# Kernel optimization log

Hardware: AMD Instinct MI355X
Metric: run time of the kernel (lower is better)

The kernel has to match this reference:

```python
import jax, jax.numpy as jnp
import numpy as np


def setup_inputs() -> dict:
    key = jax.random.key(0)
    x = jax.random.normal(key, (16, 64, 256, 256), dtype=jnp.float32)
    return {"x": x}


def reference(x):
    # x: [B, C, H, W]
    b, c, h, w = x.shape
    # L2 norm over channel dim -> [B, 1, H, W]
    weights = jnp.sqrt(jnp.sum(x * x, axis=1, keepdims=True))
    # softmax over height (dim=2)
    weights = jax.nn.softmax(weights, axis=2)
    # weighted sum over height -> [B, C, 1, W]
    weighted_sum = jnp.sum(x * weights, axis=2, keepdims=True)
    weight_sum = jnp.sum(weights, axis=2, keepdims=True)  # [B, 1, 1, W]
    compressed = weighted_sum / (weight_sum + 1e-8)
    # broadcast-repeat along height -> [B, C, H, W]
    out = jnp.broadcast_to(compressed, (b, c, h, w))
    return out
```

## Files before the change

kernel.cpp:

```cpp
#include <hip/hip_runtime.h>


constexpr int B = 16, C = 64, H = 256, W = 256, W4 = 64;
constexpr int HC = 32;
constexpr int HPC = H / HC;
constexpr float KSUB = 8.0f;

typedef float nfloat4 __attribute__((ext_vector_type(4)));

__device__ __forceinline__ float4 f4add(float4 a, float4 b) {
    return make_float4(a.x + b.x, a.y + b.y, a.z + b.z, a.w + b.w);
}

__global__ __launch_bounds__(512, 4) void k_pass1(const float* __restrict__ x,
                                                  float4* __restrict__ pcomp,
                                                  float4* __restrict__ pden) {
    __shared__ float4 red[2][8][64];
    int blk = blockIdx.x;
    int b = blk >> 5, hc = blk & 31;
    int t = threadIdx.x, cg = t >> 6, w4 = t & 63;
    int h0 = hc * HPC;

    const float4* xb = (const float4*)x + ((size_t)(b * C + cg * 8) * H + h0) * W4 + w4;

    float4 acc[8];
#pragma unroll
    for (int j = 0; j < 8; ++j) acc[j] = make_float4(0.f, 0.f, 0.f, 0.f);
    float4 dacc = make_float4(0.f, 0.f, 0.f, 0.f);

    for (int hh = 0; hh < HPC; ++hh) {
        float4 xv[8];
        float4 ps = make_float4(0.f, 0.f, 0.f, 0.f);
#pragma unroll
        for (int j = 0; j < 8; ++j) {
            xv[j] = xb[(size_t)j * H * W4 + (size_t)hh * W4];
            ps.x += xv[j].x * xv[j].x; ps.y += xv[j].y * xv[j].y;
            ps.z += xv[j].z * xv[j].z; ps.w += xv[j].w * xv[j].w;
        }
        red[hh & 1][cg][w4] = ps;
        __syncthreads();
        float4 s = make_float4(0.f, 0.f, 0.f, 0.f);
#pragma unroll
        for (int g = 0; g < 8; ++g) s = f4add(s, red[hh & 1][g][w4]);
        float4 e = make_float4(__expf(sqrtf(s.x) - KSUB), __expf(sqrtf(s.y) - KSUB),
                               __expf(sqrtf(s.z) - KSUB), __expf(sqrtf(s.w) - KSUB));
        if (cg == 0) dacc = f4add(dacc, e);
#pragma unroll
        for (int j = 0; j < 8; ++j) {
            acc[j].x += xv[j].x * e.x; acc[j].y += xv[j].y * e.y;
            acc[j].z += xv[j].z * e.z; acc[j].w += xv[j].w * e.w;
        }
    }

    size_t pc = ((size_t)(b * HC + hc) * C + cg * 8) * W4 + w4;
#pragma unroll
    for (int j = 0; j < 8; ++j)
        pcomp[pc + (size_t)j * W4] = acc[j];
    if (cg == 0)
        pden[(size_t)(b * HC + hc) * W4 + w4] = dacc;
}

__global__ __launch_bounds__(256) void k_pass2(const float4* __restrict__ pcomp,
                                               const float4* __restrict__ pden,
                                               float* __restrict__ out) {
    __shared__ float4 redc[4][64], redd[4][64];
    int blk = blockIdx.x;
    int b = blk >> 6, c = blk & 63;
    int t = threadIdx.x, hq = t >> 6, w4 = t & 63;

    float4 sc = make_float4(0.f, 0.f, 0.f, 0.f), sd = sc;
#pragma unroll
    for (int k = 0; k < 8; ++k) {
        int hc = hq * 8 + k;
        sc = f4add(sc, pcomp[((size_t)(b * HC + hc) * C + c) * W4 + w4]);
        sd = f4add(sd, pden[(size_t)(b * HC + hc) * W4 + w4]);
    }
    redc[hq][w4] = sc;
    redd[hq][w4] = sd;
    __syncthreads();
    float4 Cs = f4add(f4add(redc[0][w4], redc[1][w4]), f4add(redc[2][w4], redc[3][w4]));
    float4 Ds = f4add(f4add(redd[0][w4], redd[1][w4]), f4add(redd[2][w4], redd[3][w4]));
    nfloat4 f = { Cs.x / (Ds.x * (1.0f + 1e-8f)),
                  Cs.y / (Ds.y * (1.0f + 1e-8f)),
                  Cs.z / (Ds.z * (1.0f + 1e-8f)),
                  Cs.w / (Ds.w * (1.0f + 1e-8f)) };
    nfloat4* op = (nfloat4*)out + (size_t)(b * C + c) * H * W4;
    for (int i = t; i < H * W4; i += 256)
        __builtin_nontemporal_store(f, op + i);
}

extern "C" void kernel_launch(void* const* d_in, const int* in_sizes, int n_in,
                              void* d_out, int out_size, void* d_ws, size_t ws_size,
                              hipStream_t stream) {
    const float* x = (const float*)d_in[0];
    float* out = (float*)d_out;
    float4* pcomp = (float4*)d_ws;
    float4* pden  = pcomp + (size_t)B * HC * C * W4;

    k_pass1<<<B * HC, 512, 0, stream>>>(x, pcomp, pden);
    k_pass2<<<B * C,  256, 0, stream>>>(pcomp, pden, out);
}
```

Baseline: 456.8 us.

## Replace LDS channel reduction with wave shuffles and unroll height loop

Remaps threads in the first pass so each wavefront covers all 64 channels (as 8 channel groups of 8) for 8 float4 columns, letting the channel-sum of squares be reduced with xor shuffles instead of shared memory plus a block barrier each row. The height loop is fully unrolled to issue more loads ahead. This removes per-row __syncthreads stalls but changes the load pattern to 128-byte contiguous chunks per channel and drops the occupancy hint in launch bounds.

```diff
diff --git a/kernel.cpp b/kernel.cpp
--- a/kernel.cpp
+++ b/kernel.cpp
@@ -12,39 +12,48 @@
     return make_float4(a.x + b.x, a.y + b.y, a.z + b.z, a.w + b.w);
 }
 
-__global__ __launch_bounds__(512, 4) void k_pass1(const float* __restrict__ x,
-                                                  float4* __restrict__ pcomp,
-                                                  float4* __restrict__ pden) {
-    __shared__ float4 red[2][8][64];
+__global__ __launch_bounds__(512) void k_pass1(const float* __restrict__ x,
+                                               float4* __restrict__ pcomp,
+                                               float4* __restrict__ pden) {
     int blk = blockIdx.x;
     int b = blk >> 5, hc = blk & 31;
-    int t = threadIdx.x, cg = t >> 6, w4 = t & 63;
+    int t = threadIdx.x;
+    int lane = t & 63, wave = t >> 6;
+    int c8 = lane >> 3;
+    int w8 = lane & 7;
+    int w4 = wave * 8 + w8;
     int h0 = hc * HPC;
 
-    const float4* xb = (const float4*)x + ((size_t)(b * C + cg * 8) * H + h0) * W4 + w4;
+    const float4* xb = (const float4*)x + ((size_t)(b * C + c8) * H + h0) * W4 + w4;
+    constexpr size_t CSTRIDE = (size_t)8 * H * W4;
 
     float4 acc[8];
 #pragma unroll
     for (int j = 0; j < 8; ++j) acc[j] = make_float4(0.f, 0.f, 0.f, 0.f);
     float4 dacc = make_float4(0.f, 0.f, 0.f, 0.f);
 
+#pragma unroll
     for (int hh = 0; hh < HPC; ++hh) {
         float4 xv[8];
+#pragma unroll
+        for (int j = 0; j < 8; ++j)
+            xv[j] = xb[(size_t)j * CSTRIDE + (size_t)hh * W4];
         float4 ps = make_float4(0.f, 0.f, 0.f, 0.f);
 #pragma unroll
         for (int j = 0; j < 8; ++j) {
-            xv[j] = xb[(size_t)j * H * W4 + (size_t)hh * W4];
             ps.x += xv[j].x * xv[j].x; ps.y += xv[j].y * xv[j].y;
             ps.z += xv[j].z * xv[j].z; ps.w += xv[j].w * xv[j].w;
         }
-        red[hh & 1][cg][w4] = ps;
-        __syncthreads();
-        float4 s = make_float4(0.f, 0.f, 0.f, 0.f);
 #pragma unroll
-        for (int g = 0; g < 8; ++g) s = f4add(s, red[hh & 1][g][w4]);
-        float4 e = make_float4(__expf(sqrtf(s.x) - KSUB), __expf(sqrtf(s.y) - KSUB),
-                               __expf(sqrtf(s.z) - KSUB), __expf(sqrtf(s.w) - KSUB));
-        if (cg == 0) dacc = f4add(dacc, e);
+        for (int m = 8; m <= 32; m <<= 1) {
+            ps.x += __shfl_xor(ps.x, m);
+            ps.y += __shfl_xor(ps.y, m);
+            ps.z += __shfl_xor(ps.z, m);
+            ps.w += __shfl_xor(ps.w, m);
+        }
+        float4 e = make_float4(__expf(sqrtf(ps.x) - KSUB), __expf(sqrtf(ps.y) - KSUB),
+                               __expf(sqrtf(ps.z) - KSUB), __expf(sqrtf(ps.w) - KSUB));
+        dacc = f4add(dacc, e);
 #pragma unroll
         for (int j = 0; j < 8; ++j) {
             acc[j].x += xv[j].x * e.x; acc[j].y += xv[j].y * e.y;
@@ -52,11 +61,11 @@
         }
     }
 
-    size_t pc = ((size_t)(b * HC + hc) * C + cg * 8) * W4 + w4;
+    size_t pc = ((size_t)(b * HC + hc) * C + c8) * W4 + w4;
 #pragma unroll
     for (int j = 0; j < 8; ++j)
-        pcomp[pc + (size_t)j * W4] = acc[j];
-    if (cg == 0)
+        pcomp[pc + (size_t)(8 * j) * W4] = acc[j];
+    if (c8 == 0)
         pden[(size_t)(b * HC + hc) * W4 + w4] = dacc;
 }
 
```

Result: no change. 463.7 us (+1.5%).

## Fuse two passes into one kernel with per-batch atomic counter barrier

Applied to the files above, without the earlier changes.

Merges the partial-reduction pass and the finalize/broadcast pass into a single kernel. Blocks of the same batch signal completion through an atomic counter and spin-wait until all 32 chunks are done, then each block reduces and writes two channels of output. This removes the second launch and the gap between kernels, but adds a memset, spin-waiting, and a reliance on all 512 blocks being resident at once to avoid deadlock.

```diff
diff --git a/kernel.cpp b/kernel.cpp
--- a/kernel.cpp
+++ b/kernel.cpp
@@ -12,81 +12,98 @@
     return make_float4(a.x + b.x, a.y + b.y, a.z + b.z, a.w + b.w);
 }
 
-__global__ __launch_bounds__(512, 4) void k_pass1(const float* __restrict__ x,
-                                                  float4* __restrict__ pcomp,
-                                                  float4* __restrict__ pden) {
+__global__ __launch_bounds__(512, 4) void k_main(const float* __restrict__ x,
+                                                 float4* __restrict__ pcomp,
+                                                 float4* __restrict__ pden,
+                                                 int* __restrict__ done,
+                                                 float* __restrict__ out) {
     __shared__ float4 red[2][8][64];
     int blk = blockIdx.x;
     int b = blk >> 5, hc = blk & 31;
     int t = threadIdx.x, cg = t >> 6, w4 = t & 63;
     int h0 = hc * HPC;
 
-    const float4* xb = (const float4*)x + ((size_t)(b * C + cg * 8) * H + h0) * W4 + w4;
+    {
+        const float4* xb = (const float4*)x + ((size_t)(b * C + cg * 8) * H + h0) * W4 + w4;
+        float4 acc[8];
+#pragma unroll
+        for (int j = 0; j < 8; ++j) acc[j] = make_float4(0.f, 0.f, 0.f, 0.f);
+        float4 dacc = make_float4(0.f, 0.f, 0.f, 0.f);
 
-    float4 acc[8];
+        for (int hh = 0; hh < HPC; ++hh) {
+            float4 xv[8];
+            float4 ps = make_float4(0.f, 0.f, 0.f, 0.f);
 #pragma unroll
-    for (int j = 0; j < 8; ++j) acc[j] = make_float4(0.f, 0.f, 0.f, 0.f);
-    float4 dacc = make_float4(0.f, 0.f, 0.f, 0.f);
+            for (int j = 0; j < 8; ++j) {
+                xv[j] = xb[(size_t)j * H * W4 + (size_t)hh * W4];
+                ps.x += xv[j].x * xv[j].x; ps.y += xv[j].y * xv[j].y;
+                ps.z += xv[j].z * xv[j].z; ps.w += xv[j].w * xv[j].w;
+            }
+            red[hh & 1][cg][w4] = ps;
+            __syncthreads();
+            float4 s = make_float4(0.f, 0.f, 0.f, 0.f);
+#pragma unroll
+            for (int g = 0; g < 8; ++g) s = f4add(s, red[hh & 1][g][w4]);
+            float4 e = make_float4(__expf(sqrtf(s.x) - KSUB), __expf(sqrtf(s.y) - KSUB),
+                                   __expf(sqrtf(s.z) - KSUB), __expf(sqrtf(s.w) - KSUB));
+            if (cg == 0) dacc = f4add(dacc, e);
+#pragma unroll
+            for (int j = 0; j < 8; ++j) {
+                acc[j].x += xv[j].x * e.x; acc[j].y += xv[j].y * e.y;
+                acc[j].z += xv[j].z * e.z; acc[j].w += xv[j].w * e.w;
+            }
+        }
 
-    for (int hh = 0; hh < HPC; ++hh) {
-        float4 xv[8];
-        float4 ps = make_float4(0.f, 0.f, 0.f, 0.f);
+        size_t pc = ((size_t)(b * HC + hc) * C + cg * 8) * W4 + w4;
 #pragma unroll
-        for (int j = 0; j < 8; ++j) {
-            xv[j] = xb[(size_t)j * H * W4 + (size_t)hh * W4];
-            ps.x += xv[j].x * xv[j].x; ps.y += xv[j].y * xv[j].y;
-            ps.z += xv[j].z * xv[j].z; ps.w += xv[j].w * xv[j].w;
-        }
-        red[hh & 1][cg][w4] = ps;
-        __syncthreads();
-        float4 s = make_float4(0.f, 0.f, 0.f, 0.f);
-#pragma unroll
-        for (int g = 0; g < 8; ++g) s = f4add(s, red[hh & 1][g][w4]);
-        float4 e = make_float4(__expf(sqrtf(s.x) - KSUB), __expf(sqrtf(s.y) - KSUB),
-                               __expf(sqrtf(s.z) - KSUB), __expf(sqrtf(s.w) - KSUB));
-        if (cg == 0) dacc = f4add(dacc, e);
-#pragma unroll
-        for (int j = 0; j < 8; ++j) {
-            acc[j].x += xv[j].x * e.x; acc[j].y += xv[j].y * e.y;
-            acc[j].z += xv[j].z * e.z; acc[j].w += xv[j].w * e.w;
-        }
+        for (int j = 0; j < 8; ++j)
+            pcomp[pc + (size_t)j * W4] = acc[j];
+        if (cg == 0)
+            pden[(size_t)(b * HC + hc) * W4 + w4] = dacc;
     }
 
-    size_t pc = ((size_t)(b * HC + hc) * C + cg * 8) * W4 + w4;
+    __syncthreads();
+    if (t == 0) {
+        __threadfence();
+        __hip_atomic_fetch_add(&done[b], 1, __ATOMIC_RELEASE, __HIP_MEMORY_SCOPE_AGENT);
+        while (__hip_atomic_load(&done[b], __ATOMIC_ACQUIRE, __HIP_MEMORY_SCOPE_AGENT) < HC)
+            __builtin_amdgcn_s_sleep(8);
+        __threadfence();
+    }
+    __syncthreads();
+
+    int hg = t >> 6;
+    float4 sd = make_float4(0.f, 0.f, 0.f, 0.f);
 #pragma unroll
-    for (int j = 0; j < 8; ++j)
-        pcomp[pc + (size_t)j * W4] = acc[j];
-    if (cg == 0)
-        pden[(size_t)(b * HC + hc) * W4 + w4] = dacc;
-}
+    for (int k = 0; k < 4; ++k)
+        sd = f4add(sd, pden[(size_t)(b * HC + hg * 4 + k) * W4 + w4]);
+    red[1][hg][w4] = sd;
 
-__global__ __launch_bounds__(256) void k_pass2(const float4* __restrict__ pcomp,
-                                               const float4* __restrict__ pden,
-                                               float* __restrict__ out) {
-    __shared__ float4 redc[4][64], redd[4][64];
-    int blk = blockIdx.x;
-    int b = blk >> 6, c = blk & 63;
-    int t = threadIdx.x, hq = t >> 6, w4 = t & 63;
-
-    float4 sc = make_float4(0.f, 0.f, 0.f, 0.f), sd = sc;
 #pragma unroll
-    for (int k = 0; k < 8; ++k) {
-        int hc = hq * 8 + k;
-        sc = f4add(sc, pcomp[((size_t)(b * HC + hc) * C + c) * W4 + w4]);
-        sd = f4add(sd, pden[(size_t)(b * HC + hc) * W4 + w4]);
+    for (int ci = 0; ci < 2; ++ci) {
+        int cc = hc * 2 + ci;
+        float4 sc = make_float4(0.f, 0.f, 0.f, 0.f);
+#pragma unroll
+        for (int k = 0; k < 4; ++k)
+            sc = f4add(sc, pcomp[((size_t)(b * HC + hg * 4 + k) * C + cc) * W4 + w4]);
+        red[0][hg][w4] = sc;
+        __syncthreads();
+        float4 Cs = make_float4(0.f, 0.f, 0.f, 0.f), Ds = Cs;
+#pragma unroll
+        for (int g = 0; g < 8; ++g) {
+            Cs = f4add(Cs, red[0][g][w4]);
+            Ds = f4add(Ds, red[1][g][w4]);
+        }
+        __syncthreads();
+        nfloat4 f = { Cs.x / (Ds.x * (1.0f + 1e-8f)),
+                      Cs.y / (Ds.y * (1.0f + 1e-8f)),
+                      Cs.z / (Ds.z * (1.0f + 1e-8f)),
+                      Cs.w / (Ds.w * (1.0f + 1e-8f)) };
+        nfloat4* op = (nfloat4*)out + (size_t)(b * C + cc) * H * W4;
+#pragma unroll
+        for (int i = 0; i < 32; ++i)
+            __builtin_nontemporal_store(f, op + (size_t)i * 512 + t);
     }
-    redc[hq][w4] = sc;
-    redd[hq][w4] = sd;
-    __syncthreads();
-    float4 Cs = f4add(f4add(redc[0][w4], redc[1][w4]), f4add(redc[2][w4], redc[3][w4]));
-    float4 Ds = f4add(f4add(redd[0][w4], redd[1][w4]), f4add(redd[2][w4], redd[3][w4]));
-    nfloat4 f = { Cs.x / (Ds.x * (1.0f + 1e-8f)),
-                  Cs.y / (Ds.y * (1.0f + 1e-8f)),
-                  Cs.z / (Ds.z * (1.0f + 1e-8f)),
-                  Cs.w / (Ds.w * (1.0f + 1e-8f)) };
-    nfloat4* op = (nfloat4*)out + (size_t)(b * C + c) * H * W4;
-    for (int i = t; i < H * W4; i += 256)
-        __builtin_nontemporal_store(f, op + i);
 }
 
 extern "C" void kernel_launch(void* const* d_in, const int* in_sizes, int n_in,
@@ -96,7 +113,8 @@
     float* out = (float*)d_out;
     float4* pcomp = (float4*)d_ws;
     float4* pden  = pcomp + (size_t)B * HC * C * W4;
+    int*    done  = (int*)(pden + (size_t)B * HC * W4);
 
-    k_pass1<<<B * HC, 512, 0, stream>>>(x, pcomp, pden);
-    k_pass2<<<B * C,  256, 0, stream>>>(pcomp, pden, out);
+    hipMemsetAsync(done, 0, B * sizeof(int), stream);
+    k_main<<<B * HC, 512, 0, stream>>>(x, pcomp, pden, done, out);
 }
```

Result: slower. 572.6 us (+25.4%).
